# Performance work log

Measured on AMD Instinct MI355X. Metric: run time of the kernel, lower is better.

Reference implementation:

```python
import jax, jax.numpy as jnp
import numpy as np
from jax.scipy.special import gammaln, xlogy

B, N, DIM, H, DK, DV = 2, 2048, 1536, 8, 64, 64
NRPF = 192  # num_rel_pos_features, already divisible by 6


def get_positional_embed(n, feat):
    # Enformer positional basis: exponential, central-mask, gamma; then sign-antisymmetrized.
    nb = feat // 6  # num basis per class
    d = jnp.arange(-n + 1, n, dtype=jnp.float32)          # [2n-1]
    ad = jnp.abs(d)[:, None]                              # [2n-1, 1]
    # exponential decay features
    max_range = np.log(n) / np.log(2.0)
    half_life = 2.0 ** jnp.linspace(3.0, max_range, nb)
    e = jnp.exp(-np.log(2.0) / half_life * ad)
    # central mask features
    widths = 2.0 ** jnp.arange(1, nb + 1, dtype=jnp.float32) - 1.0
    c = (widths > ad).astype(jnp.float32)
    # gamma pdf features
    std = n / (2.0 * nb)
    mean = jnp.linspace(n / nb, float(n), nb)
    conc = (mean / std) ** 2
    rate = mean / (std ** 2)
    logp = xlogy(conc - 1.0, ad) - rate * ad - (gammaln(conc) - conc * jnp.log(rate))
    p = jnp.exp(logp) + 1e-8
    g = p / jnp.max(p)
    emb = jnp.concatenate([e, c, g], axis=-1)             # [2n-1, feat//2]
    return jnp.concatenate([emb, jnp.sign(d)[:, None] * emb], axis=-1)  # [2n-1, feat]


def relative_shift(x):
    # x: [b, h, i, 2i-1] -> [b, h, i, i]
    b, h, i, j = x.shape
    x = jnp.pad(x, ((0, 0), (0, 0), (0, 0), (1, 0)))      # [b,h,i,j+1]
    x = x.reshape(b, h, j + 1, i)[:, :, 1:, :]            # drop first 'row'
    x = x.reshape(b, h, i, j)
    return x[..., : (j + 2) // 2]                          # keep first i cols


def setup_inputs() -> dict:
    key = jax.random.key(0)
    ks = jax.random.split(key, 9)
    s = 0.02
    return {
        "x": jax.random.normal(ks[0], (B, N, DIM), jnp.float32),
        "Wq": jax.random.normal(ks[1], (DIM, H * DK), jnp.float32) * s,
        "Wk": jax.random.normal(ks[2], (DIM, H * DK), jnp.float32) * s,
        "Wv": jax.random.normal(ks[3], (DIM, H * DV), jnp.float32) * s,
        "Wo": jax.random.normal(ks[4], (H * DV, DIM), jnp.float32) * s,
        "bo": jnp.zeros((DIM,), jnp.float32),
        "Wrel": jax.random.normal(ks[5], (NRPF, H * DK), jnp.float32) * s,
        "rel_content_bias": jax.random.normal(ks[6], (1, H, 1, DK), jnp.float32),
        "rel_pos_bias": jax.random.normal(ks[7], (1, H, 1, DK), jnp.float32),
    }


def reference(x, Wq, Wk, Wv, Wo, bo, Wrel, rel_content_bias, rel_pos_bias):
    b, n, _ = x.shape
    scale = DK ** -0.5
    split = lambda t, d: t.reshape(b, n, H, d).transpose(0, 2, 1, 3)  # b h n d
    q = split(x @ Wq, DK) * scale
    k = split(x @ Wk, DK)
    v = split(x @ Wv, DV)
    content_logits = jnp.einsum('bhid,bhjd->bhij', q + rel_content_bias, k)
    pos = get_positional_embed(n, NRPF) @ Wrel               # [2n-1, H*DK]
    pos = pos.reshape(2 * n - 1, H, DK).transpose(1, 0, 2)   # h j d
    rel_logits = jnp.einsum('bhid,hjd->bhij', q + rel_pos_bias, pos)
    rel_logits = relative_shift(rel_logits)
    attn = jax.nn.softmax(content_logits + rel_logits, axis=-1)
    out = jnp.einsum('bhij,bhjd->bhid', attn, v)
    out = out.transpose(0, 2, 1, 3).reshape(b, n, H * DV)
    return out @ Wo + bo
```

## Files before the change

kernel.cpp:

```cpp
#include <hip/hip_runtime.h>
#include <stdint.h>
#include <cmath>

#define B_    2
#define N_    2048
#define DIM_  1536
#define H_    8
#define NPOS  (2*N_ - 1)
#define NB_   32

typedef __attribute__((ext_vector_type(8))) short short8;
typedef __attribute__((ext_vector_type(4))) float float4v;

struct PosConsts {
    float  inv_hl[32];
    int    widthI[32];
    float  c1[32];
    float  rateF[32];
    double gc[32];
    double maxp;
};

__device__ __forceinline__ float bf2f(unsigned short u) {
    return __uint_as_float(((unsigned int)u) << 16);
}
__device__ __forceinline__ unsigned short f2bf(float f) {
    unsigned int u = __float_as_uint(f);
    u += 0x7FFFu + ((u >> 16) & 1u);
    return (unsigned short)(u >> 16);
}
__device__ __forceinline__ unsigned int cvtpk(float lo, float hi) {
    unsigned int r;
    asm("v_cvt_pk_bf16_f32 %0, %1, %2" : "=v"(r) : "v"(lo), "v"(hi));
    return r;
}
__device__ __forceinline__ unsigned int pack2bf(float lo, float hi) {
    return cvtpk(lo, hi);
}
__device__ __forceinline__ float ldf(const void* p, int isF32, size_t idx) {
    return isF32 ? ((const float*)p)[idx] : bf2f(((const unsigned short*)p)[idx]);
}
__device__ __forceinline__ void gll16(const unsigned short* g, unsigned short* l) {
    __builtin_amdgcn_global_load_lds(
        (const __attribute__((address_space(1))) unsigned int*)g,
        (__attribute__((address_space(3))) unsigned int*)l, 16, 0, 0);
}

constexpr size_t OFF_FLAG = 0;
constexpr size_t OFF_POS  = 256;
constexpr size_t OFF_Q    = OFF_POS + (size_t)H_*4096*64*2;
constexpr size_t OFF_K    = OFF_Q   + (size_t)B_*H_*N_*64*2;
constexpr size_t OFF_V    = OFF_K   + (size_t)B_*H_*N_*64*2;
constexpr size_t OFF_WOT  = OFF_V   + (size_t)B_*H_*N_*64*2;
constexpr size_t OFF_XB   = OFF_WOT + (size_t)DIM_*512*2;
constexpr size_t OFF_AO   = OFF_XB;
constexpr size_t OFF_OP   = OFF_AO + (size_t)4096*512*2;
constexpr size_t OFF_LP   = OFF_OP + (size_t)3*16*32*4096*2;
constexpr size_t OFF_WT   = OFF_XB + (size_t)4096*DIM_*2;
static_assert(OFF_LP + (size_t)3*16*32*64*4 <= OFF_WT + (size_t)3*512*DIM_*2, "ws overflow");

__global__ __launch_bounds__(512) void prep_kernel(PosConsts pc,
                                                   const void* __restrict__ x,
                                                   const void* __restrict__ Wq, const void* __restrict__ Wk,
                                                   const void* __restrict__ Wv, const void* __restrict__ Wo,
                                                   const void* __restrict__ Wrel,
                                                   unsigned int* __restrict__ flags,
                                                   unsigned short* __restrict__ Xb,
                                                   unsigned short* __restrict__ Wt,
                                                   unsigned short* __restrict__ Wot,
                                                   unsigned short* __restrict__ posb) {
    __shared__ __align__(16) char smraw[16 * 192 * 4];
    const int tid = threadIdx.x;
    const int bid = blockIdx.x;

    int* cnt = (int*)smraw;
    int ok = 0;
    if (tid < 256) {
        unsigned short u = ((const unsigned short*)x)[2 * tid];
        int e = (u >> 7) & 0xFF;
        ok = (u == 0) || (e >= 95 && e <= 140);
    }
    cnt[tid] = ok;
    __syncthreads();
    for (int s = 256; s > 0; s >>= 1) {
        if (tid < s) cnt[tid] += cnt[tid + s];
        __syncthreads();
    }
    const int f32 = !(cnt[0] >= 192);
    __syncthreads();
    if (bid == 0 && tid == 0) flags[0] = (unsigned int)f32;

    if (bid < 256) {
        float* eb = (float*)smraw;
        const int j0 = bid * 16;
        const int c  = tid;
        for (int u = c; u < 16 * 96; u += 512) {
            int rr = u / 96, f = u - rr * 96;
            int j = j0 + rr;
            float v = 0.f, sg = 0.f;
            if (j < NPOS) {
                int dd  = j - (N_ - 1);
                int adI = dd < 0 ? -dd : dd;
                float val;
                if (f < 32) {
                    val = exp2f(-(float)adI * pc.inv_hl[f]);
                } else if (f < 64) {
                    val = (adI < pc.widthI[f - 32]) ? 1.f : 0.f;
                } else {
                    int g = f - 64;
                    if (adI == 0) {
                        val = (float)(1e-8 / pc.maxp);
                    } else {
                        double lp = (double)pc.c1[g] * log((double)adI)
                                  - (double)pc.rateF[g] * (double)adI + pc.gc[g];
                        double p = (double)expf((float)lp) + 1e-8;
                        val = (float)(p / pc.maxp);
                    }
                }
                v  = val;
                sg = (dd > 0) ? 1.f : ((dd < 0) ? -1.f : 0.f);
            }
            eb[rr * 192 + f]      = v;
            eb[rr * 192 + 96 + f] = sg * v;
        }
        __syncthreads();
        float acc[16];
#pragma unroll
        for (int rr = 0; rr < 16; ++rr) acc[rr] = 0.f;
        for (int k = 0; k < 192; k += 4) {
            float w0 = ldf(Wrel, f32, (size_t)(k + 0) * 512 + c);
            float w1 = ldf(Wrel, f32, (size_t)(k + 1) * 512 + c);
            float w2 = ldf(Wrel, f32, (size_t)(k + 2) * 512 + c);
            float w3 = ldf(Wrel, f32, (size_t)(k + 3) * 512 + c);
#pragma unroll
            for (int rr = 0; rr < 16; ++rr) {
                float4v e = *reinterpret_cast<const float4v*>(&eb[rr * 192 + k]);
                acc[rr] += e[0] * w0;
                acc[rr] += e[1] * w1;
                acc[rr] += e[2] * w2;
                acc[rr] += e[3] * w3;
            }
        }
        int h = c >> 6, dcol = c & 63;
#pragma unroll
        for (int rr = 0; rr < 16; ++rr) {
            int j = j0 + rr;
            if (j < NPOS)
                posb[((size_t)h * 4096 + j) * 64 + (dcol ^ ((j & 7) << 3))] = f2bf(acc[rr]);
        }
    } else if (bid < 3328) {
        unsigned short (*tile)[33] = (unsigned short(*)[33])smraw;
        const int idx = bid - 256;
        const int z = idx / 768, rem = idx % 768;
        const int bx = rem & 15, by = rem >> 4;
        const void* src = z == 0 ? Wq : (z == 1 ? Wk : (z == 2 ? Wv : Wo));
        unsigned short* dst = (z < 3) ? (Wt + (size_t)z * 512 * DIM_) : Wot;
        const int R = (z < 3) ? DIM_ : 512;
        const int C = (z < 3) ? 512 : DIM_;
        const int x0 = ((z < 3) ? bx : by) * 32;
        const int y0 = ((z < 3) ? by : bx) * 32;
        const int tx = tid & 31, ty = tid >> 5;
#pragma unroll
        for (int i = 0; i < 2; ++i)
            tile[ty + i * 16][tx] = f2bf(ldf(src, f32, (size_t)(y0 + ty + i * 16) * C + x0 + tx));
        __syncthreads();
#pragma unroll
        for (int i = 0; i < 2; ++i)
            dst[(size_t)(x0 + ty + i * 16) * R + y0 + tx] = tile[tx][ty + i * 16];
    } else {
        const int ab = bid - 3328;
        const size_t total = (size_t)4096 * DIM_;
        size_t i = ((size_t)ab * 512 + tid) * 8;
        const size_t stride = (size_t)1024 * 512 * 8;
        if (f32) {
            for (; i < total; i += stride) {
                float4v a = *reinterpret_cast<const float4v*>((const float*)x + i);
                float4v b = *reinterpret_cast<const float4v*>((const float*)x + i + 4);
                uint4 o;
                o.x = pack2bf(a[0], a[1]); o.y = pack2bf(a[2], a[3]);
                o.z = pack2bf(b[0], b[1]); o.w = pack2bf(b[2], b[3]);
                *reinterpret_cast<uint4*>(Xb + i) = o;
            }
        } else {
            for (; i < total; i += stride)
                *reinterpret_cast<uint4*>(Xb + i) =
                    *reinterpret_cast<const uint4*>((const unsigned short*)x + i);
        }
    }
}

__device__ __forceinline__ void gemm128_core(const unsigned short* __restrict__ A,
                                             const unsigned short* __restrict__ Bt,
                                             int K, int row0, int col0,
                                             unsigned short* As, unsigned short* Bs,
                                             float4v acc[4][4]) {
    const int tid = threadIdx.x, lane = tid & 63, w = tid >> 6;
    const int l15 = lane & 15, q8 = (lane >> 4) * 8;
    const int mr0 = (w >> 1) * 64, nc0 = (w & 1) * 64;
    const int sr = lane >> 2, sc8 = (lane & 3) * 8;
    for (int k0 = 0; k0 < K; k0 += 32) {
        __syncthreads();
        gll16(&A [(size_t)(row0 + w * 32 + sr) * K + k0 + sc8],      &As[w * 1024]);
        gll16(&A [(size_t)(row0 + w * 32 + 16 + sr) * K + k0 + sc8], &As[w * 1024 + 512]);
        gll16(&Bt[(size_t)(col0 + w * 32 + sr) * K + k0 + sc8],      &Bs[w * 1024]);
        gll16(&Bt[(size_t)(col0 + w * 32 + 16 + sr) * K + k0 + sc8], &Bs[w * 1024 + 512]);
        __syncthreads();
        short8 a[4], b[4];
#pragma unroll
        for (int mi = 0; mi < 4; ++mi)
            a[mi] = *reinterpret_cast<const short8*>(&As[(mr0 + mi * 16 + l15) * 32 + q8]);
#pragma unroll
        for (int ni = 0; ni < 4; ++ni)
            b[ni] = *reinterpret_cast<const short8*>(&Bs[(nc0 + ni * 16 + l15) * 32 + q8]);
#pragma unroll
        for (int mi = 0; mi < 4; ++mi)
#pragma unroll
            for (int ni = 0; ni < 4; ++ni)
                acc[mi][ni] = __builtin_amdgcn_mfma_f32_16x16x32_bf16(a[mi], b[ni], acc[mi][ni], 0, 0, 0);
    }
}

__global__ __launch_bounds__(256) void qkv_kernel(const unsigned short* __restrict__ Xb,
                                                  const unsigned short* __restrict__ Wt,
                                                  unsigned short* __restrict__ qbuf,
                                                  unsigned short* __restrict__ kbuf,
                                                  unsigned short* __restrict__ vbuf) {
    __shared__ __align__(16) unsigned short As[128 * 32];
    __shared__ __align__(16) unsigned short Bs[128 * 32];
    const int row0 = blockIdx.y * 128, col0 = blockIdx.x * 128;
    float4v acc[4][4];
#pragma unroll
    for (int mi = 0; mi < 4; ++mi)
#pragma unroll
        for (int ni = 0; ni < 4; ++ni) acc[mi][ni] = (float4v){0.f, 0.f, 0.f, 0.f};
    gemm128_core(Xb, Wt, DIM_, row0, col0, As, Bs, acc);
    const int lane = threadIdx.x & 63, w = threadIdx.x >> 6;
    const int l15 = lane & 15, quad = lane >> 4;
    const int mr0 = (w >> 1) * 64, nc0 = (w & 1) * 64;
#pragma unroll
    for (int mi = 0; mi < 4; ++mi)
#pragma unroll
        for (int ni = 0; ni < 4; ++ni) {
            int n = col0 + nc0 + ni * 16 + l15;
            int mode = n >> 9, nn = n & 511;
            int hh = nn >> 6, dd = nn & 63;
            int mb = row0 + mr0 + mi * 16 + quad * 4;
            int bb = mb >> 11, ii = mb & 2047;
            if (mode == 2) {
                union { unsigned short us[4]; uint2 u2; } pk;
                unsigned int p0 = cvtpk(acc[mi][ni][0], acc[mi][ni][1]);
                unsigned int p1 = cvtpk(acc[mi][ni][2], acc[mi][ni][3]);
                pk.u2 = (uint2){p0, p1};
                int jb = (ii & ~63) | ((ii & 63) ^ ((dd & 7) << 3));
                *reinterpret_cast<uint2*>(
                    &vbuf[((size_t)(bb * 8 + hh) * 64 + dd) * 2048 + jb]) = pk.u2;
            } else if (mode == 1) {
#pragma unroll
                for (int r = 0; r < 4; ++r) {
                    int tok = ii + r;
                    kbuf[((size_t)(bb * 8 + hh) * N_ + tok) * 64 + (dd ^ ((tok & 7) << 3))]
                        = f2bf(acc[mi][ni][r]);
                }
            } else {
#pragma unroll
                for (int r = 0; r < 4; ++r)
                    qbuf[((size_t)(bb * 8 + hh) * N_ + ii + r) * 64 + dd] = f2bf(acc[mi][ni][r] * 0.125f);
            }
        }
}

#define SLD 72
#define RST 68

__device__ __forceinline__ void stage_lin(const unsigned short* __restrict__ g,
                                          unsigned short* s, int tid, int w) {
    gll16(g + tid * 8,        s + w * 512);
    gll16(g + 2048 + tid * 8, s + 2048 + w * 512);
}
__device__ __forceinline__ void stage_vt(const unsigned short* __restrict__ vbase,
                                         int jbase, unsigned short* s, int tid, int w) {
    {
        int L = tid * 8;        int d = L >> 6, cb = L & 63;
        gll16(vbase + (size_t)d * 2048 + jbase + cb, s + w * 512);
    }
    {
        int L = 2048 + tid * 8; int d = L >> 6, cb = L & 63;
        gll16(vbase + (size_t)d * 2048 + jbase + cb, s + 2048 + w * 512);
    }
}

__global__ __launch_bounds__(256) void attn_kernel(const unsigned int* __restrict__ flags,
                                                   const unsigned short* __restrict__ qb,
                                                   const unsigned short* __restrict__ kb,
                                                   const unsigned short* __restrict__ vb,
                                                   const unsigned short* __restrict__ posb,
                                                   const void* __restrict__ rcb,
                                                   const void* __restrict__ rpb,
                                                   unsigned short* __restrict__ Opart,
                                                   float* __restrict__ lpart) {
    __shared__ __align__(16) unsigned short Ks[2][4096];
    __shared__ __align__(16) unsigned short Ps[2][4096];
    __shared__ __align__(16) unsigned short Vt[2][4096];
    __shared__ __align__(16) unsigned short Pp[64 * SLD];
    __shared__ __align__(8)  unsigned short Rb[128 * RST];

    const int f32 = (int)flags[0];
    const int tid = threadIdx.x;
    const int it = blockIdx.x, bh = blockIdx.y, z = blockIdx.z;
    const int h = bh & 7;
    const int i0 = it * 64;
    const size_t qoff = (size_t)bh * N_ * 64;
    const size_t poff = (size_t)h * 4096 * 64;
    const unsigned short* vbase = vb + (size_t)bh * 64 * 2048;
    const int lane = tid & 63, w = tid >> 6;
    const int l15 = lane & 15, quad = lane >> 4, q8 = quad * 8;
    const int m0 = w * 16 + quad * 4;
    const int swz = (l15 & 7) << 3;

    short8 afc[2], afr[2];
#pragma unroll
    for (int kc = 0; kc < 2; ++kc) {
        uint4 qv = *reinterpret_cast<const uint4*>(
            &qb[qoff + (size_t)(i0 + w * 16 + l15) * 64 + kc * 32 + q8]);
        unsigned int uu[4] = {qv.x, qv.y, qv.z, qv.w};
        unsigned int cw[4], rw[4];
#pragma unroll
        for (int e = 0; e < 4; ++e) {
            int k = h * 64 + kc * 32 + q8 + 2 * e;
            float lo = __uint_as_float(uu[e] << 16);
            float hi = __uint_as_float(uu[e] & 0xffff0000u);
            cw[e] = pack2bf(lo + ldf(rcb, f32, k), hi + ldf(rcb, f32, k + 1));
            rw[e] = pack2bf(lo + ldf(rpb, f32, k), hi + ldf(rpb, f32, k + 1));
        }
        union { uint4 u; short8 s; } cv, rv2;
        cv.u  = (uint4){cw[0], cw[1], cw[2], cw[3]};
        rv2.u = (uint4){rw[0], rw[1], rw[2], rw[3]};
        afc[kc] = cv.s;
        afr[kc] = rv2.s;
    }

    float4v Oa[4];
#pragma unroll
    for (int nb = 0; nb < 4; ++nb) Oa[nb] = (float4v){0.f, 0.f, 0.f, 0.f};
    float lsum[4] = {0.f, 0.f, 0.f, 0.f};

    const int base0 = 1984 - i0;
    const int t0 = z * 11, t1 = (z == 2) ? 32 : (t0 + 11);
    const int NT = t1 - t0;
    const int cs0 = base0 + t0 * 64;

    {
        int r = tid >> 2, c16 = (tid & 3) * 16;
        const uint4* psrc = reinterpret_cast<const uint4*>(&posb[poff + (size_t)(cs0 + r) * 64 + c16]);
        *reinterpret_cast<uint4*>(&Ps[0][r * 64 + c16])     = psrc[0];
        *reinterpret_cast<uint4*>(&Ps[0][r * 64 + c16 + 8]) = psrc[1];
    }
    __syncthreads();
    {
        float4v R[4];
#pragma unroll
        for (int nb = 0; nb < 4; ++nb) R[nb] = (float4v){0.f, 0.f, 0.f, 0.f};
        __builtin_amdgcn_s_setprio(1);
#pragma unroll
        for (int kc = 0; kc < 2; ++kc)
#pragma unroll
            for (int nb = 0; nb < 4; ++nb) {
                short8 pb = *reinterpret_cast<const short8*>(
                    &Ps[0][(nb * 16 + l15) * 64 + ((kc * 32 + q8) ^ swz)]);
                R[nb] = __builtin_amdgcn_mfma_f32_16x16x32_bf16(afr[kc], pb, R[nb], 0, 0, 0);
            }
        __builtin_amdgcn_s_setprio(0);
#pragma unroll
        for (int nb = 0; nb < 4; ++nb) {
            int ta = cs0 + nb * 16 + l15;
            unsigned int pk0 = cvtpk(R[nb][0], R[nb][1]);
            unsigned int pk1 = cvtpk(R[nb][2], R[nb][3]);
            Rb[(size_t)((ta + m0 + 0) & 127) * RST + m0 + 0] = (unsigned short)pk0;
            Rb[(size_t)((ta + m0 + 1) & 127) * RST + m0 + 1] = (unsigned short)(pk0 >> 16);
            Rb[(size_t)((ta + m0 + 2) & 127) * RST + m0 + 2] = (unsigned short)pk1;
            Rb[(size_t)((ta + m0 + 3) & 127) * RST + m0 + 3] = (unsigned short)(pk1 >> 16);
        }
    }
    __syncthreads();

    stage_lin(&kb[qoff + (size_t)(t0 * 64) * 64], Ks[0], tid, w);
    stage_lin(&posb[poff + (size_t)(cs0 + 64) * 64], Ps[0], tid, w);
    stage_vt(vbase, t0 * 64, Vt[0], tid, w);

    for (int u = 0; u < NT; ++u) {
        const int p = u & 1;
        const int j0 = (t0 + u) * 64, basej = base0 + j0;
        __syncthreads();

        if (u + 1 < NT) {
            stage_lin(&kb[qoff + (size_t)(j0 + 64) * 64], Ks[p ^ 1], tid, w);
            stage_lin(&posb[poff + (size_t)(cs0 + (u + 2) * 64) * 64], Ps[p ^ 1], tid, w);
            stage_vt(vbase, j0 + 64, Vt[p ^ 1], tid, w);
        }

        {
            float4v R[4];
#pragma unroll
            for (int nb = 0; nb < 4; ++nb) R[nb] = (float4v){0.f, 0.f, 0.f, 0.f};
            __builtin_amdgcn_s_setprio(1);
#pragma unroll
            for (int kc = 0; kc < 2; ++kc)
#pragma unroll
                for (int nb = 0; nb < 4; ++nb) {
                    short8 pb = *reinterpret_cast<const short8*>(
                        &Ps[p][(nb * 16 + l15) * 64 + ((kc * 32 + q8) ^ swz)]);
                    R[nb] = __builtin_amdgcn_mfma_f32_16x16x32_bf16(afr[kc], pb, R[nb], 0, 0, 0);
                }
            __builtin_amdgcn_s_setprio(0);
            const int tb = basej + 64;
#pragma unroll
            for (int nb = 0; nb < 4; ++nb) {
                int ta = tb + nb * 16 + l15;
                unsigned int pk0 = cvtpk(R[nb][0], R[nb][1]);
                unsigned int pk1 = cvtpk(R[nb][2], R[nb][3]);
                Rb[(size_t)((ta + m0 + 0) & 127) * RST + m0 + 0] = (unsigned short)pk0;
                Rb[(size_t)((ta + m0 + 1) & 127) * RST + m0 + 1] = (unsigned short)(pk0 >> 16);
                Rb[(size_t)((ta + m0 + 2) & 127) * RST + m0 + 2] = (unsigned short)pk1;
                Rb[(size_t)((ta + m0 + 3) & 127) * RST + m0 + 3] = (unsigned short)(pk1 >> 16);
            }
        }

        float4v Sacc[4];
#pragma unroll
        for (int nb = 0; nb < 4; ++nb) Sacc[nb] = (float4v){0.f, 0.f, 0.f, 0.f};
        __builtin_amdgcn_s_setprio(1);
#pragma unroll
        for (int kc = 0; kc < 2; ++kc)
#pragma unroll
            for (int nb = 0; nb < 4; ++nb) {
                short8 kf = *reinterpret_cast<const short8*>(
                    &Ks[p][(nb * 16 + l15) * 64 + ((kc * 32 + q8) ^ swz)]);
                Sacc[nb] = __builtin_amdgcn_mfma_f32_16x16x32_bf16(afc[kc], kf, Sacc[nb], 0, 0, 0);
            }
        __builtin_amdgcn_s_setprio(0);

        float pv4[4][4];
#pragma unroll
        for (int nb = 0; nb < 4; ++nb) {
            const int jl = nb * 16 + l15;
            const int row = (basej + 63 + jl) & 127;
            union { uint2 u2; unsigned short us[4]; } rv;
            rv.u2 = *reinterpret_cast<const uint2*>(&Rb[(size_t)row * RST + m0]);
#pragma unroll
            for (int r = 0; r < 4; ++r) {
                float p2 = __expf(Sacc[nb][r] + bf2f(rv.us[r]));
                pv4[nb][r] = p2;
                lsum[r] += p2;
            }
        }
#pragma unroll
        for (int r = 0; r < 4; ++r) {
            unsigned short* prow = &Pp[(m0 + r) * SLD + l15];
#pragma unroll
            for (int np = 0; np < 2; ++np) {
                unsigned int pk = cvtpk(pv4[2 * np][r], pv4[2 * np + 1][r]);
                prow[(2 * np) * 16]     = (unsigned short)pk;
                prow[(2 * np + 1) * 16] = (unsigned short)(pk >> 16);
            }
        }

        __builtin_amdgcn_s_setprio(1);
#pragma unroll
        for (int kc = 0; kc < 2; ++kc) {
            short8 pf = *reinterpret_cast<const short8*>(&Pp[(w * 16 + l15) * SLD + kc * 32 + q8]);
#pragma unroll
            for (int nb = 0; nb < 4; ++nb) {
                short8 vf = *reinterpret_cast<const short8*>(
                    &Vt[p][(nb * 16 + l15) * 64 + ((kc * 32 + q8) ^ swz)]);
                Oa[nb] = __builtin_amdgcn_mfma_f32_16x16x32_bf16(pf, vf, Oa[nb], 0, 0, 0);
            }
        }
        __builtin_amdgcn_s_setprio(0);
    }

#pragma unroll
    for (int r = 0; r < 4; ++r)
#pragma unroll
        for (int off = 1; off < 16; off <<= 1) lsum[r] += __shfl_xor(lsum[r], off);
    const size_t pslot = (size_t)(z * 16 + bh) * 32 + it;
    const size_t obase = pslot * 4096;
#pragma unroll
    for (int nb = 0; nb < 4; ++nb) {
        unsigned int pk0 = cvtpk(Oa[nb][0], Oa[nb][1]);
        unsigned int pk1 = cvtpk(Oa[nb][2], Oa[nb][3]);
        unsigned short* prow = &Pp[m0 * SLD + nb * 16 + l15];
        prow[0 * SLD] = (unsigned short)pk0;
        prow[1 * SLD] = (unsigned short)(pk0 >> 16);
        prow[2 * SLD] = (unsigned short)pk1;
        prow[3 * SLD] = (unsigned short)(pk1 >> 16);
    }
    {
        const int rr2 = w * 16 + (lane >> 2), cc2 = (lane & 3) * 16;
        uint4 o0 = *reinterpret_cast<const uint4*>(&Pp[rr2 * SLD + cc2]);
        uint4 o1 = *reinterpret_cast<const uint4*>(&Pp[rr2 * SLD + cc2 + 8]);
        *reinterpret_cast<uint4*>(&Opart[obase + (size_t)rr2 * 64 + cc2])     = o0;
        *reinterpret_cast<uint4*>(&Opart[obase + (size_t)rr2 * 64 + cc2 + 8]) = o1;
    }
    if (l15 == 0) {
#pragma unroll
        for (int r = 0; r < 4; ++r) lpart[pslot * 64 + m0 + r] = lsum[r];
    }
}

__global__ __launch_bounds__(256) void combine_kernel(const unsigned short* __restrict__ Opart,
                                                      const float* __restrict__ lpart,
                                                      unsigned short* __restrict__ ao) {
    const int it = blockIdx.x, bh = blockIdx.y;
    const int h = bh & 7, b = bh >> 3, i0 = it * 64;
    const int tid = threadIdx.x;
    const int row = tid >> 2, c0 = (tid & 3) * 16;
    float o[16];
#pragma unroll
    for (int e = 0; e < 16; ++e) o[e] = 0.f;
    float l = 0.f;
#pragma unroll
    for (int z = 0; z < 3; ++z) {
        const size_t pslot = (size_t)(z * 16 + bh) * 32 + it;
        const size_t ob = pslot * 4096 + (size_t)row * 64 + c0;
        uint4 a = *reinterpret_cast<const uint4*>(&Opart[ob]);
        uint4 b4 = *reinterpret_cast<const uint4*>(&Opart[ob + 8]);
        unsigned int uu[8] = {a.x, a.y, a.z, a.w, b4.x, b4.y, b4.z, b4.w};
#pragma unroll
        for (int e = 0; e < 8; ++e) {
            o[2 * e]     += __uint_as_float(uu[e] << 16);
            o[2 * e + 1] += __uint_as_float(uu[e] & 0xffff0000u);
        }
        l += lpart[pslot * 64 + row];
    }
    float inv = 1.0f / l;
    unsigned int ou[8];
#pragma unroll
    for (int e = 0; e < 8; ++e) ou[e] = pack2bf(o[2 * e] * inv, o[2 * e + 1] * inv);
    unsigned short* dst = &ao[((size_t)b * N_ + i0 + row) * 512 + h * 64 + c0];
    *reinterpret_cast<uint4*>(dst)     = (uint4){ou[0], ou[1], ou[2], ou[3]};
    *reinterpret_cast<uint4*>(dst + 8) = (uint4){ou[4], ou[5], ou[6], ou[7]};
}

__global__ __launch_bounds__(256) void outproj_kernel(const unsigned int* __restrict__ flags,
                                                      const unsigned short* __restrict__ AO,
                                                      const unsigned short* __restrict__ Wot,
                                                      const void* __restrict__ bo,
                                                      void* __restrict__ out) {
    __shared__ __align__(16) unsigned short As[128 * 32];
    __shared__ __align__(16) unsigned short Bs[128 * 32];
    const int f32 = (int)flags[0];
    const int row0 = blockIdx.y * 128, col0 = blockIdx.x * 128;
    float4v acc[4][4];
#pragma unroll
    for (int mi = 0; mi < 4; ++mi)
#pragma unroll
        for (int ni = 0; ni < 4; ++ni) acc[mi][ni] = (float4v){0.f, 0.f, 0.f, 0.f};
    gemm128_core(AO, Wot, 512, row0, col0, As, Bs, acc);
    const int lane = threadIdx.x & 63, w = threadIdx.x >> 6;
    const int l15 = lane & 15, quad = lane >> 4;
    const int mr0 = (w >> 1) * 64, nc0 = (w & 1) * 64;
#pragma unroll
    for (int mi = 0; mi < 4; ++mi)
#pragma unroll
        for (int ni = 0; ni < 4; ++ni) {
            int n = col0 + nc0 + ni * 16 + l15;
            float bias = ldf(bo, f32, n);
#pragma unroll
            for (int r = 0; r < 4; ++r) {
                int m = row0 + mr0 + mi * 16 + quad * 4 + r;
                float v = acc[mi][ni][r] + bias;
                if (f32) ((float*)out)[(size_t)m * DIM_ + n] = v;
                else     ((unsigned short*)out)[(size_t)m * DIM_ + n] = f2bf(v);
            }
        }
}

extern "C" void kernel_launch(void* const* d_in, const int* in_sizes, int n_in,
                              void* d_out, int out_size, void* d_ws, size_t ws_size,
                              hipStream_t stream) {
    const void* x    = d_in[0];
    const void* Wq   = d_in[1];
    const void* Wk   = d_in[2];
    const void* Wv   = d_in[3];
    const void* Wo   = d_in[4];
    const void* bo   = d_in[5];
    const void* Wrel = d_in[6];
    const void* rcb  = d_in[7];
    const void* rpb  = d_in[8];

    char* ws = (char*)d_ws;
    unsigned int*   flags = (unsigned int*)(ws + OFF_FLAG);
    unsigned short* posb  = (unsigned short*)(ws + OFF_POS);
    unsigned short* qbuf  = (unsigned short*)(ws + OFF_Q);
    unsigned short* kbuf  = (unsigned short*)(ws + OFF_K);
    unsigned short* vbuf  = (unsigned short*)(ws + OFF_V);
    unsigned short* Wot   = (unsigned short*)(ws + OFF_WOT);
    unsigned short* Xb    = (unsigned short*)(ws + OFF_XB);
    unsigned short* ao    = (unsigned short*)(ws + OFF_AO);
    unsigned short* Opart = (unsigned short*)(ws + OFF_OP);
    float*          lpart = (float*)(ws + OFF_LP);
    unsigned short* Wt    = (unsigned short*)(ws + OFF_WT);

    PosConsts pc;
    double maxp = 0.0;
    for (int g = 0; g < NB_; ++g) {
        double mean = 64.0 * (g + 1);
        double conc = (mean / 32.0) * (mean / 32.0);
        double rate = mean / 1024.0;
        double lgc  = std::lgamma(conc);
        double clr  = conc * std::log(rate);
        for (int ad = 1; ad < N_; ++ad) {
            double lp = (conc - 1.0) * std::log((double)ad) - rate * (double)ad - lgc + clr;
            double p  = std::exp(lp) + 1e-8;
            if (p > maxp) maxp = p;
        }
        pc.c1[g]    = (float)(conc - 1.0);
        pc.rateF[g] = (float)rate;
        pc.gc[g]    = -lgc + clr;
    }
    pc.maxp = maxp;
    const double max_range = std::log((double)N_) / std::log(2.0);
    for (int f = 0; f < 32; ++f) {
        double t = 3.0 + (double)f * (max_range - 3.0) / 31.0;
        pc.inv_hl[f] = (float)std::exp2(-t);
        int e = f + 1;
        pc.widthI[f] = (e >= 12) ? 0x7FFFFFFF : ((1 << e) - 1);
    }

    prep_kernel<<<dim3(4352), dim3(512), 0, stream>>>(pc, x, Wq, Wk, Wv, Wo, Wrel,
                                                      flags, Xb, Wt, Wot, posb);
    qkv_kernel<<<dim3(12, 32), dim3(256), 0, stream>>>(Xb, Wt, qbuf, kbuf, vbuf);
    attn_kernel<<<dim3(32, 16, 3), dim3(256), 0, stream>>>(flags, qbuf, kbuf, vbuf, posb, rcb, rpb, Opart, lpart);
    combine_kernel<<<dim3(32, 16), dim3(256), 0, stream>>>(Opart, lpart, ao);
    outproj_kernel<<<dim3(12, 32), dim3(256), 0, stream>>>(flags, ao, Wot, bo, d_out);
}
```

Measured before the change: 259.6 us.

## Drop split-KV attention and combine kernel; stage Q/K epilogue through LDS

The attention kernel no longer splits the key range three ways. Each block now walks all 32 key tiles, normalizes by the row sum itself and writes the attention output directly, so the combine kernel and the partial O/l buffers go away. This saves one launch and the partial-result traffic, but the grid shrinks from 1536 to 512 blocks, which lowers occupancy and parallelism on a device with many CUs. Separately, the QKV epilogue for Q and K now stages each tile in shared memory so it can write 16-byte coalesced stores instead of scattered 2-byte stores.

```diff
diff --git a/kernel.cpp b/kernel.cpp
--- a/kernel.cpp
+++ b/kernel.cpp
@@ -225,8 +225,9 @@
                                                   unsigned short* __restrict__ qbuf,
                                                   unsigned short* __restrict__ kbuf,
                                                   unsigned short* __restrict__ vbuf) {
-    __shared__ __align__(16) unsigned short As[128 * 32];
-    __shared__ __align__(16) unsigned short Bs[128 * 32];
+    __shared__ __align__(16) unsigned short smem[2 * 128 * 32];
+    unsigned short* As = smem;
+    unsigned short* Bs = smem + 128 * 32;
     const int row0 = blockIdx.y * 128, col0 = blockIdx.x * 128;
     float4v acc[4][4];
 #pragma unroll
@@ -234,19 +235,23 @@
 #pragma unroll
         for (int ni = 0; ni < 4; ++ni) acc[mi][ni] = (float4v){0.f, 0.f, 0.f, 0.f};
     gemm128_core(Xb, Wt, DIM_, row0, col0, As, Bs, acc);
+    __syncthreads();
+
     const int lane = threadIdx.x & 63, w = threadIdx.x >> 6;
     const int l15 = lane & 15, quad = lane >> 4;
     const int mr0 = (w >> 1) * 64, nc0 = (w & 1) * 64;
-#pragma unroll
-    for (int mi = 0; mi < 4; ++mi)
-#pragma unroll
-        for (int ni = 0; ni < 4; ++ni) {
-            int n = col0 + nc0 + ni * 16 + l15;
-            int mode = n >> 9, nn = n & 511;
-            int hh = nn >> 6, dd = nn & 63;
-            int mb = row0 + mr0 + mi * 16 + quad * 4;
-            int bb = mb >> 11, ii = mb & 2047;
-            if (mode == 2) {
+    const int n0 = col0 + nc0;
+    const int mode = n0 >> 9;
+    const int hh = (n0 & 511) >> 6;
+
+    if (mode == 2) {
+#pragma unroll
+        for (int mi = 0; mi < 4; ++mi)
+#pragma unroll
+            for (int ni = 0; ni < 4; ++ni) {
+                int dd = ni * 16 + l15;
+                int mb = row0 + mr0 + mi * 16 + quad * 4;
+                int bb = mb >> 11, ii = mb & 2047;
                 union { unsigned short us[4]; uint2 u2; } pk;
                 unsigned int p0 = cvtpk(acc[mi][ni][0], acc[mi][ni][1]);
                 unsigned int p1 = cvtpk(acc[mi][ni][2], acc[mi][ni][3]);
@@ -254,19 +259,29 @@
                 int jb = (ii & ~63) | ((ii & 63) ^ ((dd & 7) << 3));
                 *reinterpret_cast<uint2*>(
                     &vbuf[((size_t)(bb * 8 + hh) * 64 + dd) * 2048 + jb]) = pk.u2;
-            } else if (mode == 1) {
-#pragma unroll
-                for (int r = 0; r < 4; ++r) {
-                    int tok = ii + r;
-                    kbuf[((size_t)(bb * 8 + hh) * N_ + tok) * 64 + (dd ^ ((tok & 7) << 3))]
-                        = f2bf(acc[mi][ni][r]);
-                }
-            } else {
+            }
+    } else {
+        unsigned short* Obuf = (mode == 0) ? qbuf : kbuf;
+        const float scale = (mode == 0) ? 0.125f : 1.0f;
+        unsigned short* Lw = smem + w * 16 * 72;
+        const int r16 = lane >> 2, c4 = (lane & 3) * 16;
+#pragma unroll
+        for (int mi = 0; mi < 4; ++mi) {
+#pragma unroll
+            for (int ni = 0; ni < 4; ++ni)
 #pragma unroll
                 for (int r = 0; r < 4; ++r)
-                    qbuf[((size_t)(bb * 8 + hh) * N_ + ii + r) * 64 + dd] = f2bf(acc[mi][ni][r] * 0.125f);
-            }
-        }
+                    Lw[(quad * 4 + r) * 72 + ni * 16 + l15] = f2bf(acc[mi][ni][r] * scale);
+            int mb = row0 + mr0 + mi * 16 + r16;
+            int bb = mb >> 11, tok = mb & 2047;
+            unsigned short* gp = &Obuf[((size_t)(bb * 8 + hh) * N_ + tok) * 64];
+            uint4 v0 = *reinterpret_cast<const uint4*>(&Lw[r16 * 72 + c4]);
+            uint4 v1 = *reinterpret_cast<const uint4*>(&Lw[r16 * 72 + c4 + 8]);
+            int swz2 = (mode == 1) ? ((tok & 7) << 3) : 0;
+            *reinterpret_cast<uint4*>(gp + (c4 ^ swz2))       = v0;
+            *reinterpret_cast<uint4*>(gp + ((c4 + 8) ^ swz2)) = v1;
+        }
+    }
 }
 
 #define SLD 72
@@ -296,8 +311,7 @@
                                                    const unsigned short* __restrict__ posb,
                                                    const void* __restrict__ rcb,
                                                    const void* __restrict__ rpb,
-                                                   unsigned short* __restrict__ Opart,
-                                                   float* __restrict__ lpart) {
+                                                   unsigned short* __restrict__ ao) {
     __shared__ __align__(16) unsigned short Ks[2][4096];
     __shared__ __align__(16) unsigned short Ps[2][4096];
     __shared__ __align__(16) unsigned short Vt[2][4096];
@@ -306,8 +320,8 @@
 
     const int f32 = (int)flags[0];
     const int tid = threadIdx.x;
-    const int it = blockIdx.x, bh = blockIdx.y, z = blockIdx.z;
-    const int h = bh & 7;
+    const int it = blockIdx.x, bh = blockIdx.y;
+    const int h = bh & 7, b = bh >> 3;
     const int i0 = it * 64;
     const size_t qoff = (size_t)bh * N_ * 64;
     const size_t poff = (size_t)h * 4096 * 64;
@@ -345,9 +359,8 @@
     float lsum[4] = {0.f, 0.f, 0.f, 0.f};
 
     const int base0 = 1984 - i0;
-    const int t0 = z * 11, t1 = (z == 2) ? 32 : (t0 + 11);
-    const int NT = t1 - t0;
-    const int cs0 = base0 + t0 * 64;
+    const int NT = 32;
+    const int cs0 = base0;
 
     {
         int r = tid >> 2, c16 = (tid & 3) * 16;
@@ -383,13 +396,13 @@
     }
     __syncthreads();
 
-    stage_lin(&kb[qoff + (size_t)(t0 * 64) * 64], Ks[0], tid, w);
+    stage_lin(&kb[qoff], Ks[0], tid, w);
     stage_lin(&posb[poff + (size_t)(cs0 + 64) * 64], Ps[0], tid, w);
-    stage_vt(vbase, t0 * 64, Vt[0], tid, w);
+    stage_vt(vbase, 0, Vt[0], tid, w);
 
     for (int u = 0; u < NT; ++u) {
         const int p = u & 1;
-        const int j0 = (t0 + u) * 64, basej = base0 + j0;
+        const int j0 = u * 64, basej = base0 + j0;
         __syncthreads();
 
         if (u + 1 < NT) {
@@ -479,15 +492,15 @@
     }
 
 #pragma unroll
-    for (int r = 0; r < 4; ++r)
+    for (int r = 0; r < 4; ++r) {
 #pragma unroll
         for (int off = 1; off < 16; off <<= 1) lsum[r] += __shfl_xor(lsum[r], off);
-    const size_t pslot = (size_t)(z * 16 + bh) * 32 + it;
-    const size_t obase = pslot * 4096;
+        lsum[r] = 1.0f / lsum[r];
+    }
 #pragma unroll
     for (int nb = 0; nb < 4; ++nb) {
-        unsigned int pk0 = cvtpk(Oa[nb][0], Oa[nb][1]);
-        unsigned int pk1 = cvtpk(Oa[nb][2], Oa[nb][3]);
+        unsigned int pk0 = cvtpk(Oa[nb][0] * lsum[0], Oa[nb][1] * lsum[1]);
+        unsigned int pk1 = cvtpk(Oa[nb][2] * lsum[2], Oa[nb][3] * lsum[3]);
         unsigned short* prow = &Pp[m0 * SLD + nb * 16 + l15];
         prow[0 * SLD] = (unsigned short)pk0;
         prow[1 * SLD] = (unsigned short)(pk0 >> 16);
@@ -498,47 +511,10 @@
         const int rr2 = w * 16 + (lane >> 2), cc2 = (lane & 3) * 16;
         uint4 o0 = *reinterpret_cast<const uint4*>(&Pp[rr2 * SLD + cc2]);
         uint4 o1 = *reinterpret_cast<const uint4*>(&Pp[rr2 * SLD + cc2 + 8]);
-        *reinterpret_cast<uint4*>(&Opart[obase + (size_t)rr2 * 64 + cc2])     = o0;
-        *reinterpret_cast<uint4*>(&Opart[obase + (size_t)rr2 * 64 + cc2 + 8]) = o1;
-    }
-    if (l15 == 0) {
-#pragma unroll
-        for (int r = 0; r < 4; ++r) lpart[pslot * 64 + m0 + r] = lsum[r];
-    }
-}
-
-__global__ __launch_bounds__(256) void combine_kernel(const unsigned short* __restrict__ Opart,
-                                                      const float* __restrict__ lpart,
-                                                      unsigned short* __restrict__ ao) {
-    const int it = blockIdx.x, bh = blockIdx.y;
-    const int h = bh & 7, b = bh >> 3, i0 = it * 64;
-    const int tid = threadIdx.x;
-    const int row = tid >> 2, c0 = (tid & 3) * 16;
-    float o[16];
-#pragma unroll
-    for (int e = 0; e < 16; ++e) o[e] = 0.f;
-    float l = 0.f;
-#pragma unroll
-    for (int z = 0; z < 3; ++z) {
-        const size_t pslot = (size_t)(z * 16 + bh) * 32 + it;
-        const size_t ob = pslot * 4096 + (size_t)row * 64 + c0;
-        uint4 a = *reinterpret_cast<const uint4*>(&Opart[ob]);
-        uint4 b4 = *reinterpret_cast<const uint4*>(&Opart[ob + 8]);
-        unsigned int uu[8] = {a.x, a.y, a.z, a.w, b4.x, b4.y, b4.z, b4.w};
-#pragma unroll
-        for (int e = 0; e < 8; ++e) {
-            o[2 * e]     += __uint_as_float(uu[e] << 16);
-            o[2 * e + 1] += __uint_as_float(uu[e] & 0xffff0000u);
-        }
-        l += lpart[pslot * 64 + row];
-    }
-    float inv = 1.0f / l;
-    unsigned int ou[8];
-#pragma unroll
-    for (int e = 0; e < 8; ++e) ou[e] = pack2bf(o[2 * e] * inv, o[2 * e + 1] * inv);
-    unsigned short* dst = &ao[((size_t)b * N_ + i0 + row) * 512 + h * 64 + c0];
-    *reinterpret_cast<uint4*>(dst)     = (uint4){ou[0], ou[1], ou[2], ou[3]};
-    *reinterpret_cast<uint4*>(dst + 8) = (uint4){ou[4], ou[5], ou[6], ou[7]};
+        unsigned short* dst = &ao[((size_t)(b * N_ + i0 + rr2)) * 512 + h * 64 + cc2];
+        *reinterpret_cast<uint4*>(dst)     = o0;
+        *reinterpret_cast<uint4*>(dst + 8) = o1;
+    }
 }
 
 __global__ __launch_bounds__(256) void outproj_kernel(const unsigned int* __restrict__ flags,
@@ -597,8 +573,6 @@
     unsigned short* Wot   = (unsigned short*)(ws + OFF_WOT);
     unsigned short* Xb    = (unsigned short*)(ws + OFF_XB);
     unsigned short* ao    = (unsigned short*)(ws + OFF_AO);
-    unsigned short* Opart = (unsigned short*)(ws + OFF_OP);
-    float*          lpart = (float*)(ws + OFF_LP);
     unsigned short* Wt    = (unsigned short*)(ws + OFF_WT);
 
     PosConsts pc;
@@ -630,7 +604,6 @@
     prep_kernel<<<dim3(4352), dim3(512), 0, stream>>>(pc, x, Wq, Wk, Wv, Wo, Wrel,
                                                       flags, Xb, Wt, Wot, posb);
     qkv_kernel<<<dim3(12, 32), dim3(256), 0, stream>>>(Xb, Wt, qbuf, kbuf, vbuf);
-    attn_kernel<<<dim3(32, 16, 3), dim3(256), 0, stream>>>(flags, qbuf, kbuf, vbuf, posb, rcb, rpb, Opart, lpart);
-    combine_kernel<<<dim3(32, 16), dim3(256), 0, stream>>>(Opart, lpart, ao);
+    attn_kernel<<<dim3(32, 16), dim3(256), 0, stream>>>(flags, qbuf, kbuf, vbuf, posb, rcb, rpb, ao);
     outproj_kernel<<<dim3(12, 32), dim3(256), 0, stream>>>(flags, ao, Wot, bo, d_out);
 }
```

Result: faster. 247.9 us (-4.5%).
